# Performance work log

Hardware: AMD Instinct MI355X
Metric: run time of the kernel (lower is better)

Reference implementation:

```python
import jax, jax.numpy as jnp
import numpy as np

C = 128          # inchannel
CH = C // 2      # projected channels
N_, D_, H_, W_ = 2, 16, 16, 16


def setup_inputs() -> dict:
    key = jax.random.key(0)
    kx, kq, kk, kv, kp = jax.random.split(key, 5)
    s_in = 1.0 / np.sqrt(C)
    s_mid = 1.0 / np.sqrt(CH)
    return {
        "x": jax.random.normal(kx, (N_, C, D_, H_, W_), dtype=jnp.float32),
        "Wq": jax.random.normal(kq, (CH, C), dtype=jnp.float32) * s_in,
        "Wk": jax.random.normal(kk, (CH, C), dtype=jnp.float32) * s_in,
        "Wv": jax.random.normal(kv, (CH, C), dtype=jnp.float32) * s_in,
        "Wpost": jax.random.normal(kp, (C, CH), dtype=jnp.float32) * s_mid,
    }


def reference(x, Wq, Wk, Wv, Wpost):
    n, c_in, d, h, w = x.shape
    npos = d * h * w
    xf = x.reshape(n, c_in, npos)                     # (n, C, N)
    # 1x1x1 conv3d (no bias) == channel-mixing matmul
    q = jnp.einsum('oc,ncx->nox', Wq, xf)             # (n, CH, N)
    k = jnp.einsum('oc,ncx->nox', Wk, xf)             # (n, CH, N)
    v = jnp.einsum('oc,ncx->nox', Wv, xf)             # (n, CH, N)
    # atten_map[b,i,j] = sum_c k[b,c,i] * q[b,c,j], softmax over j (dim=2)
    scores = jnp.einsum('nci,ncj->nij', k, q)         # (n, N, N)
    attn = jax.nn.softmax(scores, axis=2)
    # val @ attn: out[b,c,j] = sum_i v[b,c,i] * attn[b,i,j]
    agg = jnp.einsum('nci,nij->ncj', v, attn)         # (n, CH, N)
    post = jnp.einsum('oc,ncx->nox', Wpost, agg)      # (n, C, N)
    return post.reshape(n, c_in, d, h, w) + x
```

## Files before the change

### kernel.cpp

```cpp
#include <hip/hip_runtime.h>
#include <math.h>

#define NB   2
#define CIN  128
#define CH   64
#define NPOS 4096

typedef __attribute__((ext_vector_type(8))) short s16x8;
typedef __attribute__((ext_vector_type(4))) float f32x4;

__device__ __forceinline__ unsigned int bfrne(float f) {
    unsigned int u = __float_as_uint(f);
    return (u + 0x7FFFu + ((u >> 16) & 1u)) >> 16;
}
__device__ __forceinline__ unsigned int pk_rne(float lo, float hi) {
    return bfrne(lo) | (bfrne(hi) << 16);
}
__device__ __forceinline__ unsigned int pk_fast(float lo, float hi) {
    unsigned int a = (__float_as_uint(lo) + 0x8000u) >> 16;
    unsigned int b = (__float_as_uint(hi) + 0x8000u) & 0xFFFF0000u;
    return a | b;
}
__device__ __forceinline__ float bf2f(unsigned short h) {
    return __uint_as_float(((unsigned int)h) << 16);
}

__global__ __launch_bounds__(256) void packw_kernel(
    const float* __restrict__ Wq, const float* __restrict__ Wk,
    const float* __restrict__ Wv, const float* __restrict__ Wpost,
    unsigned short* __restrict__ Wb)
{
    const int gid = blockIdx.x * 256 + threadIdx.x;
    const int base = gid * 4;
    const int mat = base >> 13, off = base & 8191;
    const float* src = (mat == 0) ? Wq : (mat == 1) ? Wk : (mat == 2) ? Wv : Wpost;
    float4 f = *(const float4*)&src[off];
    uint2 st = make_uint2(pk_rne(f.x, f.y), pk_rne(f.z, f.w));
    *(uint2*)&Wb[mat * 8192 + off] = st;
}

#define XTS 132
__global__ __launch_bounds__(256, 4) void qkv_kernel(
    const float* __restrict__ x, const unsigned short* __restrict__ Wb,
    unsigned short* __restrict__ kT, unsigned short* __restrict__ qT,
    float* __restrict__ v32)
{
    __shared__ __align__(16) float xT[16 * XTS];
    const int b  = blockIdx.z;
    const int og = blockIdx.y;
    const int p0 = blockIdx.x * 16;
    const int tid = threadIdx.x;

    #pragma unroll
    for (int it = 0; it < 2; ++it) {
        int idx = it * 256 + tid;
        int c = idx >> 2, p4 = (idx & 3) * 4;
        float4 g = *(const float4*)&x[((size_t)b * CIN + c) * NPOS + p0 + p4];
        xT[(p4 + 0) * XTS + c] = g.x;
        xT[(p4 + 1) * XTS + c] = g.y;
        xT[(p4 + 2) * XTS + c] = g.z;
        xT[(p4 + 3) * XTS + c] = g.w;
    }
    __syncthreads();

    const int w = tid >> 6, l = tid & 63, lm = l & 15, lq = l >> 4;
    const int p = p0 + lm;

    s16x8 Bhi[4], Blo[4];
    #pragma unroll
    for (int ck = 0; ck < 4; ++ck) {
        const float* xr = &xT[lm * XTS + ck * 32 + lq * 8];
        union { unsigned int u[4]; s16x8 v; } chv, clv;
        #pragma unroll
        for (int j = 0; j < 4; ++j) {
            float x0 = xr[2 * j], x1 = xr[2 * j + 1];
            unsigned int h0 = bfrne(x0), h1 = bfrne(x1);
            chv.u[j] = h0 | (h1 << 16);
            clv.u[j] = pk_rne(x0 - __uint_as_float(h0 << 16),
                              x1 - __uint_as_float(h1 << 16));
        }
        Bhi[ck] = chv.v; Blo[ck] = clv.v;
    }

    const int tile = og * 4 + w;
    const int mat = tile >> 2, o0 = (tile & 3) * 16;
    const unsigned short* Wm = Wb + mat * 8192;
    f32x4 acc = {0.f, 0.f, 0.f, 0.f};
    #pragma unroll
    for (int ck = 0; ck < 4; ++ck) {
        s16x8 aW = *(const s16x8*)&Wm[(o0 + lm) * CIN + ck * 32 + lq * 8];
        acc = __builtin_amdgcn_mfma_f32_16x16x32_bf16(aW, Bhi[ck], acc, 0,0,0);
        acc = __builtin_amdgcn_mfma_f32_16x16x32_bf16(aW, Blo[ck], acc, 0,0,0);
    }
    if (mat < 2) {
        unsigned short* dst = (mat == 0) ? qT : kT;
        uint2 st = make_uint2(pk_rne(acc[0], acc[1]), pk_rne(acc[2], acc[3]));
        *(uint2*)&dst[((size_t)b * NPOS + p) * CH + o0 + lq * 4] = st;
    } else {
        #pragma unroll
        for (int r = 0; r < 4; ++r)
            v32[((size_t)b * CH + o0 + lq * 4 + r) * NPOS + p] = acc[r];
    }
}

__global__ __launch_bounds__(256, 4) void stats_kernel(
    const unsigned short* __restrict__ kT,
    const unsigned short* __restrict__ qT,
    float* __restrict__ lpart)
{
    __shared__ __align__(16) unsigned short qbuf[2][4096];
    const int b  = blockIdx.z;
    const int jq = blockIdx.y;
    const int i0 = blockIdx.x * 64;
    const int tid = threadIdx.x;
    const int w = tid >> 6, l = tid & 63, lm = l & 15, lq = l >> 4;

    s16x8 a0 = *(const s16x8*)&kT[
        ((size_t)b * NPOS + i0 + w * 16 + lm) * CH + lq * 8];
    s16x8 a1 = *(const s16x8*)&kT[
        ((size_t)b * NPOS + i0 + w * 16 + lm) * CH + 32 + lq * 8];

    const unsigned short* qpt =
        qT + ((size_t)b * NPOS + jq * 512 + w * 16 + lm) * CH + lq * 8;
    s16x8 st0 = *(const s16x8*)(qpt);
    s16x8 st1 = *(const s16x8*)(qpt + 32);

    float rs[4] = {0.f, 0.f, 0.f, 0.f};
    for (int t = 0; t < 8; ++t) {
        const int buf = t & 1;
        *(s16x8*)&qbuf[buf][(2 * w + 0) * 512 + l * 8] = st0;
        *(s16x8*)&qbuf[buf][(2 * w + 1) * 512 + l * 8] = st1;
        if (t < 7) {
            const unsigned short* qn = qpt + (size_t)(t + 1) * 64 * CH;
            st0 = *(const s16x8*)(qn);
            st1 = *(const s16x8*)(qn + 32);
        }
        __syncthreads();
        #pragma unroll
        for (int js = 0; js < 4; ++js) {
            s16x8 b0 = *(const s16x8*)&qbuf[buf][(js * 2 + 0) * 512 + l * 8];
            s16x8 b1 = *(const s16x8*)&qbuf[buf][(js * 2 + 1) * 512 + l * 8];
            f32x4 sc = {0.f, 0.f, 0.f, 0.f};
            sc = __builtin_amdgcn_mfma_f32_16x16x32_bf16(a0, b0, sc, 0,0,0);
            sc = __builtin_amdgcn_mfma_f32_16x16x32_bf16(a1, b1, sc, 0,0,0);
            rs[0] += __expf(sc[0]); rs[1] += __expf(sc[1]);
            rs[2] += __expf(sc[2]); rs[3] += __expf(sc[3]);
        }
    }

    #pragma unroll
    for (int r = 0; r < 4; ++r) {
        rs[r] += __shfl_xor(rs[r], 1);
        rs[r] += __shfl_xor(rs[r], 2);
        rs[r] += __shfl_xor(rs[r], 4);
        rs[r] += __shfl_xor(rs[r], 8);
    }
    if (lm == 0) {
        #pragma unroll
        for (int r = 0; r < 4; ++r)
            lpart[(size_t)jq * NB * NPOS + b * NPOS
                  + i0 + w * 16 + lq * 4 + r] = rs[r];
    }
}

__global__ __launch_bounds__(256) void combine_kernel(
    const float* __restrict__ lpart, const float* __restrict__ v32,
    unsigned short* __restrict__ vbs)
{
    const int idx4 = blockIdx.x * 256 + threadIdx.x;
    const int base = idx4 * 4;
    const int b = base >> 18;
    const int i = base & (NPOS - 1);
    const float* lp = lpart + b * NPOS + i;
    float sx = 0.f, sy = 0.f, sz = 0.f, sw = 0.f;
    #pragma unroll
    for (int qq = 0; qq < 8; ++qq) {
        float4 lv = *(const float4*)(lp + (size_t)qq * NB * NPOS);
        sx += lv.x; sy += lv.y; sz += lv.z; sw += lv.w;
    }
    float4 v = *(const float4*)&v32[base];
    uint2 st = make_uint2(pk_rne(v.x / sx, v.y / sy),
                          pk_rne(v.z / sz, v.w / sw));
    *(uint2*)&vbs[base] = st;
}

__global__ __launch_bounds__(256, 4) void agg_kernel(
    const unsigned short* __restrict__ kT,
    const unsigned short* __restrict__ qT,
    const unsigned short* __restrict__ vbs,
    unsigned short* __restrict__ U)
{
    __shared__ __align__(16) unsigned short kbuf[2][2048];
    __shared__ __align__(16) unsigned short vbuf[2][2048];
    const int b  = blockIdx.z;
    const int iq = blockIdx.y;
    const int j0 = blockIdx.x * 128;
    const int tid = threadIdx.x;
    const int w = tid >> 6, l = tid & 63, lm = l & 15, lq = l >> 4;

    s16x8 qb[2][2];
    #pragma unroll
    for (int js = 0; js < 2; ++js)
        #pragma unroll
        for (int kc = 0; kc < 2; ++kc)
            qb[js][kc] = *(const s16x8*)&qT[
                ((size_t)b * NPOS + j0 + w * 32 + js * 16 + lm) * CH + kc * 32 + lq * 8];

    int addr[4];
    #pragma unroll
    for (int d = 0; d < 4; ++d)
        addr[d] = (lm + 16 * (2 * (lq & 1) + (d >> 1))) << 2;
    const bool lowhalf = (lq < 2);

    const unsigned short* kpt = kT
        + ((size_t)b * NPOS + iq * 256 + (w >> 1) * 16 + lm) * CH
        + (w & 1) * 32 + lq * 8;
    const unsigned short* vpt = vbs
        + ((size_t)b * CH + w * 16 + lm) * NPOS + iq * 256 + lq * 8;

    f32x4 acc[2][4] = {};
    s16x8 kst = *(const s16x8*)kpt;
    s16x8 vst = *(const s16x8*)vpt;

    for (int t = 0; t < 8; ++t) {
        const int buf = t & 1;
        *(s16x8*)&kbuf[buf][w * 512 + l * 8] = kst;
        *(s16x8*)&vbuf[buf][w * 512 + l * 8] = vst;
        if (t < 7) {
            kst = *(const s16x8*)(kpt + (t + 1) * 32 * CH);
            vst = *(const s16x8*)(vpt + (t + 1) * 32);
        }
        __syncthreads();

        s16x8 kA[2][2], vA[4];
        #pragma unroll
        for (int s = 0; s < 2; ++s)
            #pragma unroll
            for (int kc = 0; kc < 2; ++kc)
                kA[s][kc] = *(const s16x8*)&kbuf[buf][(s * 2 + kc) * 512 + l * 8];
        #pragma unroll
        for (int cs = 0; cs < 4; ++cs)
            vA[cs] = *(const s16x8*)&vbuf[buf][cs * 512 + l * 8];

        #pragma unroll
        for (int js = 0; js < 2; ++js) {
            f32x4 s0 = {0,0,0,0}, s1 = {0,0,0,0};
            s0 = __builtin_amdgcn_mfma_f32_16x16x32_bf16(kA[0][0], qb[js][0], s0, 0,0,0);
            s0 = __builtin_amdgcn_mfma_f32_16x16x32_bf16(kA[0][1], qb[js][1], s0, 0,0,0);
            s1 = __builtin_amdgcn_mfma_f32_16x16x32_bf16(kA[1][0], qb[js][0], s1, 0,0,0);
            s1 = __builtin_amdgcn_mfma_f32_16x16x32_bf16(kA[1][1], qb[js][1], s1, 0,0,0);

            unsigned int P0[2], P1[2];
            P0[0] = pk_fast(__expf(s0[0]), __expf(s0[1]));
            P0[1] = pk_fast(__expf(s0[2]), __expf(s0[3]));
            P1[0] = pk_fast(__expf(s1[0]), __expf(s1[1]));
            P1[1] = pk_fast(__expf(s1[2]), __expf(s1[3]));

            union { unsigned int u[4]; s16x8 v; } B;
            #pragma unroll
            for (int d = 0; d < 4; ++d) {
                int t0 = __builtin_amdgcn_ds_bpermute(addr[d], (int)P0[d & 1]);
                int t1 = __builtin_amdgcn_ds_bpermute(addr[d], (int)P1[d & 1]);
                B.u[d] = lowhalf ? (unsigned int)t0 : (unsigned int)t1;
            }
            #pragma unroll
            for (int cs = 0; cs < 4; ++cs)
                acc[js][cs] = __builtin_amdgcn_mfma_f32_16x16x32_bf16(
                    vA[cs], B.v, acc[js][cs], 0,0,0);
        }
    }

    unsigned short* Up = U + ((size_t)iq * NB + b) * NPOS * CH;
    #pragma unroll
    for (int js = 0; js < 2; ++js)
        #pragma unroll
        for (int cs = 0; cs < 4; ++cs) {
            uint2 st = make_uint2(pk_rne(acc[js][cs][0], acc[js][cs][1]),
                                  pk_rne(acc[js][cs][2], acc[js][cs][3]));
            *(uint2*)&Up[(size_t)(j0 + w * 32 + js * 16 + lm) * CH
                         + cs * 16 + lq * 4] = st;
        }
}

__global__ __launch_bounds__(256, 4) void post_kernel(
    const float* __restrict__ x, const unsigned short* __restrict__ Wb,
    const unsigned short* __restrict__ U, float* __restrict__ out)
{
    const int b  = blockIdx.y;
    const int p0 = blockIdx.x * 16;
    const int tid = threadIdx.x;
    const int w = tid >> 6, l = tid & 63, lm = l & 15, lq = l >> 4;
    const int p = p0 + lm;
    const size_t PS = (size_t)NB * NPOS * CH;

    const unsigned short* u = U + ((size_t)b * NPOS + p) * CH;
    const unsigned short* Wpb = Wb + 3 * 8192;
    s16x8 Bf[2];
    #pragma unroll
    for (int ck = 0; ck < 2; ++ck) {
        float sv[8] = {};
        #pragma unroll
        for (int qq = 0; qq < 16; ++qq) {
            union { s16x8 v; unsigned short us[8]; } uu;
            uu.v = *(const s16x8*)(u + (size_t)qq * PS + ck * 32 + lq * 8);
            #pragma unroll
            for (int j = 0; j < 8; ++j) sv[j] += bf2f(uu.us[j]);
        }
        union { unsigned int u[4]; s16x8 v; } cb;
        #pragma unroll
        for (int j = 0; j < 4; ++j) cb.u[j] = pk_rne(sv[2*j], sv[2*j+1]);
        Bf[ck] = cb.v;
    }

    #pragma unroll
    for (int ot = 0; ot < 2; ++ot) {
        const int o0 = (w * 2 + ot) * 16;
        f32x4 acc = {0.f, 0.f, 0.f, 0.f};
        #pragma unroll
        for (int ck = 0; ck < 2; ++ck) {
            s16x8 aW = *(const s16x8*)&Wpb[(o0 + lm) * CH + ck * 32 + lq * 8];
            acc = __builtin_amdgcn_mfma_f32_16x16x32_bf16(aW, Bf[ck], acc, 0,0,0);
        }
        #pragma unroll
        for (int r = 0; r < 4; ++r) {
            size_t gi = ((size_t)b * CIN + o0 + lq * 4 + r) * NPOS + p;
            out[gi] = x[gi] + acc[r];
        }
    }
}

extern "C" void kernel_launch(void* const* d_in, const int* in_sizes, int n_in,
                              void* d_out, int out_size, void* d_ws, size_t ws_size,
                              hipStream_t stream) {
    const float* x     = (const float*)d_in[0];
    const float* Wq    = (const float*)d_in[1];
    const float* Wk    = (const float*)d_in[2];
    const float* Wv    = (const float*)d_in[3];
    const float* Wpost = (const float*)d_in[4];
    float* out = (float*)d_out;

    unsigned short* kT  = (unsigned short*)d_ws;
    unsigned short* qT  = kT + (size_t)NB * NPOS * CH;
    unsigned short* vbs = qT + (size_t)NB * NPOS * CH;
    unsigned short* Wb  = vbs + (size_t)NB * NPOS * CH;
    float* lpart = (float*)(Wb + 4 * 8192);
    unsigned short* U = (unsigned short*)(lpart + (size_t)8 * NB * NPOS);
    float* v32 = (float*)U;

    packw_kernel  <<<dim3(32), 256, 0, stream>>>(Wq, Wk, Wv, Wpost, Wb);
    qkv_kernel    <<<dim3(NPOS / 16, 3, NB), 256, 0, stream>>>(x, Wb, kT, qT, v32);
    stats_kernel  <<<dim3(NPOS / 64, 8, NB), 256, 0, stream>>>(kT, qT, lpart);
    combine_kernel<<<dim3(NB * CH * NPOS / 1024), 256, 0, stream>>>(lpart, v32, vbs);
    agg_kernel    <<<dim3(NPOS / 128, 16, NB), 256, 0, stream>>>(kT, qT, vbs, U);
    post_kernel   <<<dim3(NPOS / 16, NB), 256, 0, stream>>>(x, Wb, U, out);
}
```

Before: 118.5 us.

## Fold softmax normalization into agg, fuse QKV tiles, halve i-split partials

```diff
diff --git a/kernel.cpp b/kernel.cpp
--- a/kernel.cpp
+++ b/kernel.cpp
@@ -40,14 +40,13 @@
 }
 
 #define XTS 132
-__global__ __launch_bounds__(256, 4) void qkv_kernel(
+__global__ __launch_bounds__(256) void qkv_kernel(
     const float* __restrict__ x, const unsigned short* __restrict__ Wb,
     unsigned short* __restrict__ kT, unsigned short* __restrict__ qT,
-    float* __restrict__ v32)
+    unsigned short* __restrict__ vbs)
 {
     __shared__ __align__(16) float xT[16 * XTS];
-    const int b  = blockIdx.z;
-    const int og = blockIdx.y;
+    const int b  = blockIdx.y;
     const int p0 = blockIdx.x * 16;
     const int tid = threadIdx.x;
 
@@ -82,24 +81,28 @@
         Bhi[ck] = chv.v; Blo[ck] = clv.v;
     }
 
-    const int tile = og * 4 + w;
-    const int mat = tile >> 2, o0 = (tile & 3) * 16;
-    const unsigned short* Wm = Wb + mat * 8192;
-    f32x4 acc = {0.f, 0.f, 0.f, 0.f};
-    #pragma unroll
-    for (int ck = 0; ck < 4; ++ck) {
-        s16x8 aW = *(const s16x8*)&Wm[(o0 + lm) * CIN + ck * 32 + lq * 8];
-        acc = __builtin_amdgcn_mfma_f32_16x16x32_bf16(aW, Bhi[ck], acc, 0,0,0);
-        acc = __builtin_amdgcn_mfma_f32_16x16x32_bf16(aW, Blo[ck], acc, 0,0,0);
-    }
-    if (mat < 2) {
-        unsigned short* dst = (mat == 0) ? qT : kT;
-        uint2 st = make_uint2(pk_rne(acc[0], acc[1]), pk_rne(acc[2], acc[3]));
-        *(uint2*)&dst[((size_t)b * NPOS + p) * CH + o0 + lq * 4] = st;
-    } else {
-        #pragma unroll
-        for (int r = 0; r < 4; ++r)
-            v32[((size_t)b * CH + o0 + lq * 4 + r) * NPOS + p] = acc[r];
+    #pragma unroll
+    for (int t3 = 0; t3 < 3; ++t3) {
+        const int tile = w * 3 + t3;
+        const int mat = tile >> 2, o0 = (tile & 3) * 16;
+        const unsigned short* Wm = Wb + mat * 8192;
+        f32x4 acc = {0.f, 0.f, 0.f, 0.f};
+        #pragma unroll
+        for (int ck = 0; ck < 4; ++ck) {
+            s16x8 aW = *(const s16x8*)&Wm[(o0 + lm) * CIN + ck * 32 + lq * 8];
+            acc = __builtin_amdgcn_mfma_f32_16x16x32_bf16(aW, Bhi[ck], acc, 0,0,0);
+            acc = __builtin_amdgcn_mfma_f32_16x16x32_bf16(aW, Blo[ck], acc, 0,0,0);
+        }
+        if (mat < 2) {
+            unsigned short* dst = (mat == 0) ? qT : kT;
+            uint2 st = make_uint2(pk_rne(acc[0], acc[1]), pk_rne(acc[2], acc[3]));
+            *(uint2*)&dst[((size_t)b * NPOS + p) * CH + o0 + lq * 4] = st;
+        } else {
+            #pragma unroll
+            for (int r = 0; r < 4; ++r)
+                vbs[((size_t)b * CH + o0 + lq * 4 + r) * NPOS + p] =
+                    (unsigned short)bfrne(acc[r]);
+        }
     }
 }
 
@@ -163,41 +166,40 @@
     }
 }
 
-__global__ __launch_bounds__(256) void combine_kernel(
-    const float* __restrict__ lpart, const float* __restrict__ v32,
-    unsigned short* __restrict__ vbs)
+__global__ __launch_bounds__(256) void gl_kernel(
+    const float* __restrict__ lpart, float* __restrict__ gl)
 {
     const int idx4 = blockIdx.x * 256 + threadIdx.x;
     const int base = idx4 * 4;
-    const int b = base >> 18;
-    const int i = base & (NPOS - 1);
-    const float* lp = lpart + b * NPOS + i;
     float sx = 0.f, sy = 0.f, sz = 0.f, sw = 0.f;
     #pragma unroll
     for (int qq = 0; qq < 8; ++qq) {
-        float4 lv = *(const float4*)(lp + (size_t)qq * NB * NPOS);
+        float4 lv = *(const float4*)(lpart + (size_t)qq * NB * NPOS + base);
         sx += lv.x; sy += lv.y; sz += lv.z; sw += lv.w;
     }
-    float4 v = *(const float4*)&v32[base];
-    uint2 st = make_uint2(pk_rne(v.x / sx, v.y / sy),
-                          pk_rne(v.z / sz, v.w / sw));
-    *(uint2*)&vbs[base] = st;
+    float4 o = make_float4(1.f / sx, 1.f / sy, 1.f / sz, 1.f / sw);
+    *(float4*)&gl[base] = o;
 }
 
 __global__ __launch_bounds__(256, 4) void agg_kernel(
     const unsigned short* __restrict__ kT,
     const unsigned short* __restrict__ qT,
     const unsigned short* __restrict__ vbs,
+    const float* __restrict__ gl,
     unsigned short* __restrict__ U)
 {
     __shared__ __align__(16) unsigned short kbuf[2][2048];
     __shared__ __align__(16) unsigned short vbuf[2][2048];
+    __shared__ __align__(16) float rls[512];
     const int b  = blockIdx.z;
     const int iq = blockIdx.y;
     const int j0 = blockIdx.x * 128;
     const int tid = threadIdx.x;
     const int w = tid >> 6, l = tid & 63, lm = l & 15, lq = l >> 4;
 
+    *(float2*)&rls[tid * 2] =
+        *(const float2*)&gl[(size_t)b * NPOS + iq * 512 + tid * 2];
+
     s16x8 qb[2][2];
     #pragma unroll
     for (int js = 0; js < 2; ++js)
@@ -213,20 +215,20 @@
     const bool lowhalf = (lq < 2);
 
     const unsigned short* kpt = kT
-        + ((size_t)b * NPOS + iq * 256 + (w >> 1) * 16 + lm) * CH
+        + ((size_t)b * NPOS + iq * 512 + (w >> 1) * 16 + lm) * CH
         + (w & 1) * 32 + lq * 8;
     const unsigned short* vpt = vbs
-        + ((size_t)b * CH + w * 16 + lm) * NPOS + iq * 256 + lq * 8;
+        + ((size_t)b * CH + w * 16 + lm) * NPOS + iq * 512 + lq * 8;
 
     f32x4 acc[2][4] = {};
     s16x8 kst = *(const s16x8*)kpt;
     s16x8 vst = *(const s16x8*)vpt;
 
-    for (int t = 0; t < 8; ++t) {
+    for (int t = 0; t < 16; ++t) {
         const int buf = t & 1;
         *(s16x8*)&kbuf[buf][w * 512 + l * 8] = kst;
         *(s16x8*)&vbuf[buf][w * 512 + l * 8] = vst;
-        if (t < 7) {
+        if (t < 15) {
             kst = *(const s16x8*)(kpt + (t + 1) * 32 * CH);
             vst = *(const s16x8*)(vpt + (t + 1) * 32);
         }
@@ -241,6 +243,9 @@
         #pragma unroll
         for (int cs = 0; cs < 4; ++cs)
             vA[cs] = *(const s16x8*)&vbuf[buf][cs * 512 + l * 8];
+
+        f32x4 rl0 = *(const f32x4*)&rls[t * 32 + lq * 4];
+        f32x4 rl1 = *(const f32x4*)&rls[t * 32 + 16 + lq * 4];
 
         #pragma unroll
         for (int js = 0; js < 2; ++js) {
@@ -251,10 +256,10 @@
             s1 = __builtin_amdgcn_mfma_f32_16x16x32_bf16(kA[1][1], qb[js][1], s1, 0,0,0);
 
             unsigned int P0[2], P1[2];
-            P0[0] = pk_fast(__expf(s0[0]), __expf(s0[1]));
-            P0[1] = pk_fast(__expf(s0[2]), __expf(s0[3]));
-            P1[0] = pk_fast(__expf(s1[0]), __expf(s1[1]));
-            P1[1] = pk_fast(__expf(s1[2]), __expf(s1[3]));
+            P0[0] = pk_fast(__expf(s0[0]) * rl0[0], __expf(s0[1]) * rl0[1]);
+            P0[1] = pk_fast(__expf(s0[2]) * rl0[2], __expf(s0[3]) * rl0[3]);
+            P1[0] = pk_fast(__expf(s1[0]) * rl1[0], __expf(s1[1]) * rl1[1]);
+            P1[1] = pk_fast(__expf(s1[2]) * rl1[2], __expf(s1[3]) * rl1[3]);
 
             union { unsigned int u[4]; s16x8 v; } B;
             #pragma unroll
@@ -282,15 +287,16 @@
         }
 }
 
-__global__ __launch_bounds__(256, 4) void post_kernel(
+__global__ __launch_bounds__(256) void post_kernel(
     const float* __restrict__ x, const unsigned short* __restrict__ Wb,
     const unsigned short* __restrict__ U, float* __restrict__ out)
 {
     const int b  = blockIdx.y;
-    const int p0 = blockIdx.x * 16;
+    const int p0 = blockIdx.x * 32;
     const int tid = threadIdx.x;
     const int w = tid >> 6, l = tid & 63, lm = l & 15, lq = l >> 4;
-    const int p = p0 + lm;
+    const int psub = (w & 1) * 16, ohalf = w >> 1;
+    const int p = p0 + psub + lm;
     const size_t PS = (size_t)NB * NPOS * CH;
 
     const unsigned short* u = U + ((size_t)b * NPOS + p) * CH;
@@ -300,7 +306,7 @@
     for (int ck = 0; ck < 2; ++ck) {
         float sv[8] = {};
         #pragma unroll
-        for (int qq = 0; qq < 16; ++qq) {
+        for (int qq = 0; qq < 8; ++qq) {
             union { s16x8 v; unsigned short us[8]; } uu;
             uu.v = *(const s16x8*)(u + (size_t)qq * PS + ck * 32 + lq * 8);
             #pragma unroll
@@ -313,8 +319,8 @@
     }
 
     #pragma unroll
-    for (int ot = 0; ot < 2; ++ot) {
-        const int o0 = (w * 2 + ot) * 16;
+    for (int ot = 0; ot < 4; ++ot) {
+        const int o0 = (ohalf * 4 + ot) * 16;
         f32x4 acc = {0.f, 0.f, 0.f, 0.f};
         #pragma unroll
         for (int ck = 0; ck < 2; ++ck) {
@@ -344,13 +350,13 @@
     unsigned short* vbs = qT + (size_t)NB * NPOS * CH;
     unsigned short* Wb  = vbs + (size_t)NB * NPOS * CH;
     float* lpart = (float*)(Wb + 4 * 8192);
-    unsigned short* U = (unsigned short*)(lpart + (size_t)8 * NB * NPOS);
-    float* v32 = (float*)U;
-
-    packw_kernel  <<<dim3(32), 256, 0, stream>>>(Wq, Wk, Wv, Wpost, Wb);
-    qkv_kernel    <<<dim3(NPOS / 16, 3, NB), 256, 0, stream>>>(x, Wb, kT, qT, v32);
-    stats_kernel  <<<dim3(NPOS / 64, 8, NB), 256, 0, stream>>>(kT, qT, lpart);
-    combine_kernel<<<dim3(NB * CH * NPOS / 1024), 256, 0, stream>>>(lpart, v32, vbs);
-    agg_kernel    <<<dim3(NPOS / 128, 16, NB), 256, 0, stream>>>(kT, qT, vbs, U);
-    post_kernel   <<<dim3(NPOS / 16, NB), 256, 0, stream>>>(x, Wb, U, out);
-}
+    float* gl    = lpart + (size_t)8 * NB * NPOS;
+    unsigned short* U = (unsigned short*)(gl + (size_t)NB * NPOS);
+
+    packw_kernel<<<dim3(32), 256, 0, stream>>>(Wq, Wk, Wv, Wpost, Wb);
+    qkv_kernel  <<<dim3(NPOS / 16, NB), 256, 0, stream>>>(x, Wb, kT, qT, vbs);
+    stats_kernel<<<dim3(NPOS / 64, 8, NB), 256, 0, stream>>>(kT, qT, lpart);
+    gl_kernel   <<<dim3(8), 256, 0, stream>>>(lpart, gl);
+    agg_kernel  <<<dim3(NPOS / 128, 8, NB), 256, 0, stream>>>(kT, qT, vbs, gl, U);
+    post_kernel <<<dim3(NPOS / 32, NB), 256, 0, stream>>>(x, Wb, U, out);
+}
```

Measured after the change: 107.7 us. 9.2% less time.
